# Performance work log

Measured on AMD Instinct MI355X. Metric: run time of the kernel, lower is better.

The kernel has to match this reference:

```python
import jax, jax.numpy as jnp
import numpy as np

K = 2  # binary (k-ary) heap-layout tree: children of node j are K*j+1 .. K*j+K

def _levels(N):
    # level of node i in heap layout = floor(log2(i+1)); returns list of index arrays, root level first
    lev = np.floor(np.log2(np.arange(N) + 1)).astype(np.int64)
    depth = int(lev.max()) + 1
    return [np.where(lev == l)[0] for l in range(depth)]

def setup_inputs() -> dict:
    key = jax.random.key(0)
    ks = jax.random.split(key, 9)
    B, N, D = 512, 127, 300
    s = 0.05
    return {
        'x':     jax.random.normal(ks[0], (B, N, D), jnp.float32),
        'Wioux': jax.random.normal(ks[1], (D, 3 * D), jnp.float32) * s,
        'bioux': jax.random.normal(ks[2], (3 * D,), jnp.float32) * s,
        'Wiouh': jax.random.normal(ks[3], (D, 3 * D), jnp.float32) * s,
        'biouh': jax.random.normal(ks[4], (3 * D,), jnp.float32) * s,
        'Wfx':   jax.random.normal(ks[5], (D, D), jnp.float32) * s,
        'bfx':   jax.random.normal(ks[6], (D,), jnp.float32) * s,
        'Wfh':   jax.random.normal(ks[7], (D, D), jnp.float32) * s,
        'bfh':   jax.random.normal(ks[8], (D,), jnp.float32) * s,
    }

def reference(x, Wioux, bioux, Wiouh, biouh, Wfx, bfx, Wfh, bfh):
    # Child-Sum Tree-LSTM, level-synchronous (leaves -> root), batched over B trees.
    B, N, D = x.shape
    levels = _levels(N)
    H = jnp.zeros((B, N, D), x.dtype)
    C = jnp.zeros((B, N, D), x.dtype)
    for idx in reversed(levels):  # process deepest level first
        ch = idx[:, None] * K + 1 + np.arange(K)          # [n, K] child node ids (static)
        valid = jnp.asarray((ch < N), x.dtype)[None, :, :, None]  # [1,n,K,1]
        chc = np.minimum(ch, N - 1)
        ch_h = H[:, chc] * valid                           # [B,n,K,D]; padded children -> 0 (leaf case)
        ch_c = C[:, chc] * valid
        h_sum = ch_h.sum(axis=2)                           # child-sum of hidden states [B,n,D]
        xj = x[:, idx]                                     # [B,n,D]
        iou = xj @ Wioux + bioux + h_sum @ Wiouh + biouh   # [B,n,3D]
        i_g, o_g, u_g = jnp.split(iou, 3, axis=-1)
        i_g = jax.nn.sigmoid(i_g)
        o_g = jax.nn.sigmoid(o_g)
        u_g = jnp.tanh(u_g)
        fx = (xj @ Wfx + bfx)[:, :, None, :]               # broadcast over children
        f = jax.nn.sigmoid(jnp.einsum('bnkd,de->bnke', ch_h, Wfh) + bfh + fx)
        c = i_g * u_g + (f * ch_c).sum(axis=2)             # fc sum; padded ch_c==0
        h = o_g * jnp.tanh(c)
        H = H.at[:, idx].set(h)
        C = C.at[:, idx].set(c)
    return H  # per-node hidden states (contexts); root hidden = H[:, 0]
```

## Files before the change

### kernel.cpp

```cpp
#include <hip/hip_runtime.h>
#include <math.h>

#define DIM 300
#define NN 127
#define KP 320
#define MATSZ (KP*KP)

typedef short bf16x8 __attribute__((ext_vector_type(8)));
typedef float f32x16 __attribute__((ext_vector_type(16)));

__device__ __forceinline__ unsigned short f2bf(float f){
    unsigned u = __float_as_uint(f);
    u += 0x7fffu + ((u >> 16) & 1u);
    return (unsigned short)(u >> 16);
}
__device__ __forceinline__ float sigf(float v){ return 1.0f/(1.0f+__expf(-v)); }
__device__ __forceinline__ float tanh_(float v){
    float t = __expf(-2.0f*fabsf(v));
    float r = (1.0f - t)/(1.0f + t);
    return v < 0.0f ? -r : r;
}
__device__ __forceinline__ void glds16(const void* g, void* l){
    __builtin_amdgcn_global_load_lds(
        (const __attribute__((address_space(1))) unsigned int*)g,
        (__attribute__((address_space(3))) unsigned int*)l, 16, 0, 0);
}

#define MFMA __builtin_amdgcn_mfma_f32_32x32x16_bf16

__global__ void prep_weights(const float* __restrict__ Wioux,
                             const float* __restrict__ Wiouh,
                             const float* __restrict__ Wfx,
                             const float* __restrict__ Wfh,
                             unsigned short* __restrict__ WT)
{
    int k = threadIdx.x;
    int n = blockIdx.x;
    int m = blockIdx.y;
    float v = 0.f;
    if (k < DIM && n < DIM){
        if (m < 3)       v = Wioux[k*(3*DIM) + m*DIM + n];
        else if (m < 6)  v = Wiouh[k*(3*DIM) + (m-3)*DIM + n];
        else if (m == 6) v = Wfx[k*DIM + n];
        else             v = Wfh[k*DIM + n];
    }
    WT[m*MATSZ + n*KP + k] = f2bf(v);
}

__global__ __launch_bounds__(256,2)
void leaf_mfma(const float* __restrict__ x,
               const float* __restrict__ bioux, const float* __restrict__ biouh,
               const unsigned short* __restrict__ WT,
               float* __restrict__ H, float* __restrict__ C)
{
    __shared__ __attribute__((aligned(16))) short lds[10240];
    const int t = threadIdx.x, lane = t & 63, wave = t >> 6;
    const int wm = wave >> 1, wn = wave & 1;
    const int lrow = lane & 31, half = lane >> 5;
    const int rowBase = blockIdx.x * 128, d0 = blockIdx.y * 64;

    const float* aptr[2]; int adst[2]; int acg[2];
    #pragma unroll
    for (int i = 0; i < 2; i++){
        int ca = wave*2 + i;
        int r = ca*16 + (lane >> 2);
        int grow = rowBase + r;
        int b = grow >> 6, j = 63 + (grow & 63);
        int cg = (lane & 3) ^ (r & 3);
        aptr[i] = x + (b*NN + j)*DIM + cg*8;
        acg[i] = cg;
        adst[i] = ca*512 + lane*8;
    }
    const unsigned short* bptr[3]; short* bdst[3];
    #pragma unroll
    for (int i = 0; i < 3; i++){
        int cb = wave*3 + i;
        int m = cb >> 2, g = cb & 3;
        int n = g*16 + (lane >> 2);
        int cg = (lane & 3) ^ (n & 3);
        bptr[i] = WT + m*MATSZ + (d0 + n)*KP + cg*8;
        bdst[i] = lds + 4096 + cb*512;
    }

    f32x16 accI[2], accO[2], accU[2];
    #pragma unroll
    for (int rt = 0; rt < 2; rt++)
        #pragma unroll
        for (int q = 0; q < 16; q++){ accI[rt][q]=0.f; accO[rt][q]=0.f; accU[rt][q]=0.f; }

    #pragma unroll
    for (int ks = 0; ks < 10; ks++){
        #pragma unroll
        for (int i = 0; i < 3; i++) glds16(bptr[i] + ks*32, bdst[i]);
        #pragma unroll
        for (int i = 0; i < 2; i++){
            bf16x8 v;
            if ((ks+1)*32 <= DIM){
                float4 p0 = *(const float4*)(aptr[i] + ks*32);
                float4 p1 = *(const float4*)(aptr[i] + ks*32 + 4);
                v[0]=f2bf(p0.x); v[1]=f2bf(p0.y); v[2]=f2bf(p0.z); v[3]=f2bf(p0.w);
                v[4]=f2bf(p1.x); v[5]=f2bf(p1.y); v[6]=f2bf(p1.z); v[7]=f2bf(p1.w);
            } else {
                int kc = ks*32 + acg[i]*8;
                #pragma unroll
                for (int e = 0; e < 8; e++) v[e] = 0;
                if (kc + 8 <= DIM){
                    float4 p0 = *(const float4*)(aptr[i] + ks*32);
                    float4 p1 = *(const float4*)(aptr[i] + ks*32 + 4);
                    v[0]=f2bf(p0.x); v[1]=f2bf(p0.y); v[2]=f2bf(p0.z); v[3]=f2bf(p0.w);
                    v[4]=f2bf(p1.x); v[5]=f2bf(p1.y); v[6]=f2bf(p1.z); v[7]=f2bf(p1.w);
                } else if (kc < DIM){
                    float4 p0 = *(const float4*)(aptr[i] + ks*32);
                    v[0]=f2bf(p0.x); v[1]=f2bf(p0.y); v[2]=f2bf(p0.z); v[3]=f2bf(p0.w);
                }
            }
            *(bf16x8*)(lds + adst[i]) = v;
        }
        __syncthreads();
        #pragma unroll
        for (int kk = 0; kk < 2; kk++){
            int p = ((kk<<1) + half) ^ (lrow & 3);
            const short* Bb = lds + 4096 + (wn*32 + lrow)*32 + p*8;
            bf16x8 b0 = *(const bf16x8*)(Bb);
            bf16x8 b1 = *(const bf16x8*)(Bb + 2048);
            bf16x8 b2 = *(const bf16x8*)(Bb + 4096);
            const short* Ab = lds + (wm*64 + lrow)*32 + p*8;
            #pragma unroll
            for (int rt = 0; rt < 2; rt++){
                bf16x8 ax = *(const bf16x8*)(Ab + rt*1024);
                accI[rt] = MFMA(ax, b0, accI[rt], 0, 0, 0);
                accO[rt] = MFMA(ax, b1, accO[rt], 0, 0, 0);
                accU[rt] = MFMA(ax, b2, accU[rt], 0, 0, 0);
            }
        }
        __syncthreads();
    }
    int d = d0 + wn*32 + lrow;
    if (d < DIM){
        float bi  = bioux[d]       + biouh[d];
        float bo_ = bioux[DIM+d]   + biouh[DIM+d];
        float bu  = bioux[2*DIM+d] + biouh[2*DIM+d];
        #pragma unroll
        for (int rt = 0; rt < 2; rt++)
            #pragma unroll
            for (int q = 0; q < 16; q++){
                int grow = rowBase + wm*64 + rt*32 + (q&3) + 8*(q>>2) + 4*half;
                int b = grow >> 6, j = 63 + (grow & 63);
                int ob = (b*NN + j)*DIM + d;
                float iv = sigf (accI[rt][q] + bi);
                float ov = sigf (accO[rt][q] + bo_);
                float uv = tanh_(accU[rt][q] + bu);
                float cv = iv*uv;
                C[ob] = cv;
                H[ob] = ov*tanh_(cv);
            }
    }
}

__global__ __launch_bounds__(256,2)
void level_mfma(const float* __restrict__ x,
                const float* __restrict__ bioux, const float* __restrict__ biouh,
                const float* __restrict__ bfx,   const float* __restrict__ bfh,
                const unsigned short* __restrict__ WT,
                float* __restrict__ H, float* __restrict__ C,
                int lo, int lshift)
{
    __shared__ __attribute__((aligned(16))) short lds[28672];
    const int t = threadIdx.x, lane = t & 63, wave = t >> 6;
    const int wm = wave >> 1, wn = wave & 1;
    const int lrow = lane & 31, half = lane >> 5;
    const int rowBase = blockIdx.x * 128, d0 = blockIdx.y * 64;
    const int nmask = (1 << lshift) - 1;

    const float* aptr[6]; int adst[6]; int acg[6];
    #pragma unroll
    for (int i = 0; i < 6; i++){
        int ca = wave*6 + i;
        int s = ca >> 3, rg = ca & 7;
        int r = rg*16 + (lane >> 2);
        int grow = rowBase + r;
        int b = grow >> lshift, j = lo + (grow & nmask);
        int node = (s == 0) ? j : ((s == 1) ? 2*j+1 : 2*j+2);
        const float* base = (s == 0) ? x : H;
        int cg = (lane & 3) ^ (r & 3);
        aptr[i] = base + (b*NN + node)*DIM + cg*8;
        acg[i] = cg;
        adst[i] = ca*512 + lane*8;
    }
    const unsigned short* bptr[8]; short* bdst[8];
    #pragma unroll
    for (int i = 0; i < 8; i++){
        int cb = wave*8 + i;
        int m = cb >> 2, g = cb & 3;
        int n = g*16 + (lane >> 2);
        int cg = (lane & 3) ^ (n & 3);
        bptr[i] = WT + m*MATSZ + (d0 + n)*KP + cg*8;
        bdst[i] = lds + 12288 + cb*512;
    }

    f32x16 accI[2], accO[2], accU[2], accF0[2], accF1[2];
    #pragma unroll
    for (int rt = 0; rt < 2; rt++)
        #pragma unroll
        for (int q = 0; q < 16; q++){
            accI[rt][q]=0.f; accO[rt][q]=0.f; accU[rt][q]=0.f;
            accF0[rt][q]=0.f; accF1[rt][q]=0.f;
        }

    #pragma unroll
    for (int ks = 0; ks < 10; ks++){
        #pragma unroll
        for (int i = 0; i < 8; i++) glds16(bptr[i] + ks*32, bdst[i]);
        #pragma unroll
        for (int i = 0; i < 6; i++){
            bf16x8 v;
            if ((ks+1)*32 <= DIM){
                float4 p0 = *(const float4*)(aptr[i] + ks*32);
                float4 p1 = *(const float4*)(aptr[i] + ks*32 + 4);
                v[0]=f2bf(p0.x); v[1]=f2bf(p0.y); v[2]=f2bf(p0.z); v[3]=f2bf(p0.w);
                v[4]=f2bf(p1.x); v[5]=f2bf(p1.y); v[6]=f2bf(p1.z); v[7]=f2bf(p1.w);
            } else {
                int kc = ks*32 + acg[i]*8;
                #pragma unroll
                for (int e = 0; e < 8; e++) v[e] = 0;
                if (kc + 8 <= DIM){
                    float4 p0 = *(const float4*)(aptr[i] + ks*32);
                    float4 p1 = *(const float4*)(aptr[i] + ks*32 + 4);
                    v[0]=f2bf(p0.x); v[1]=f2bf(p0.y); v[2]=f2bf(p0.z); v[3]=f2bf(p0.w);
                    v[4]=f2bf(p1.x); v[5]=f2bf(p1.y); v[6]=f2bf(p1.z); v[7]=f2bf(p1.w);
                } else if (kc < DIM){
                    float4 p0 = *(const float4*)(aptr[i] + ks*32);
                    v[0]=f2bf(p0.x); v[1]=f2bf(p0.y); v[2]=f2bf(p0.z); v[3]=f2bf(p0.w);
                }
            }
            *(bf16x8*)(lds + adst[i]) = v;
        }
        __syncthreads();
        #pragma unroll
        for (int kk = 0; kk < 2; kk++){
            int p = ((kk<<1) + half) ^ (lrow & 3);
            const short* Bb = lds + 12288 + (wn*32 + lrow)*32 + p*8;
            bf16x8 b0 = *(const bf16x8*)(Bb);
            bf16x8 b1 = *(const bf16x8*)(Bb + 2048);
            bf16x8 b2 = *(const bf16x8*)(Bb + 2*2048);
            bf16x8 b3 = *(const bf16x8*)(Bb + 3*2048);
            bf16x8 b4 = *(const bf16x8*)(Bb + 4*2048);
            bf16x8 b5 = *(const bf16x8*)(Bb + 5*2048);
            bf16x8 b6 = *(const bf16x8*)(Bb + 6*2048);
            bf16x8 b7 = *(const bf16x8*)(Bb + 7*2048);
            const short* Ab = lds + (wm*64 + lrow)*32 + p*8;
            #pragma unroll
            for (int rt = 0; rt < 2; rt++){
                bf16x8 ax = *(const bf16x8*)(Ab + rt*1024);
                bf16x8 a0 = *(const bf16x8*)(Ab + 4096 + rt*1024);
                bf16x8 a1 = *(const bf16x8*)(Ab + 8192 + rt*1024);
                accI[rt]  = MFMA(ax, b0, accI[rt], 0, 0, 0);
                accI[rt]  = MFMA(a0, b3, accI[rt], 0, 0, 0);
                accI[rt]  = MFMA(a1, b3, accI[rt], 0, 0, 0);
                accO[rt]  = MFMA(ax, b1, accO[rt], 0, 0, 0);
                accO[rt]  = MFMA(a0, b4, accO[rt], 0, 0, 0);
                accO[rt]  = MFMA(a1, b4, accO[rt], 0, 0, 0);
                accU[rt]  = MFMA(ax, b2, accU[rt], 0, 0, 0);
                accU[rt]  = MFMA(a0, b5, accU[rt], 0, 0, 0);
                accU[rt]  = MFMA(a1, b5, accU[rt], 0, 0, 0);
                accF0[rt] = MFMA(ax, b6, accF0[rt], 0, 0, 0);
                accF0[rt] = MFMA(a0, b7, accF0[rt], 0, 0, 0);
                accF1[rt] = MFMA(ax, b6, accF1[rt], 0, 0, 0);
                accF1[rt] = MFMA(a1, b7, accF1[rt], 0, 0, 0);
            }
        }
        __syncthreads();
    }
    int d = d0 + wn*32 + lrow;
    if (d < DIM){
        float bi  = bioux[d]       + biouh[d];
        float bo_ = bioux[DIM+d]   + biouh[DIM+d];
        float bu  = bioux[2*DIM+d] + biouh[2*DIM+d];
        float bf_ = bfx[d] + bfh[d];
        #pragma unroll
        for (int rt = 0; rt < 2; rt++)
            #pragma unroll
            for (int q = 0; q < 16; q++){
                int grow = rowBase + wm*64 + rt*32 + (q&3) + 8*(q>>2) + 4*half;
                int b = grow >> lshift, j = lo + (grow & nmask);
                int ob  = (b*NN + j)*DIM + d;
                float c0 = C[(b*NN + 2*j+1)*DIM + d];
                float c1 = C[(b*NN + 2*j+2)*DIM + d];
                float iv = sigf (accI[rt][q] + bi);
                float ov = sigf (accO[rt][q] + bo_);
                float uv = tanh_(accU[rt][q] + bu);
                float f0 = sigf (accF0[rt][q] + bf_);
                float f1 = sigf (accF1[rt][q] + bf_);
                float cv = iv*uv + f0*c0 + f1*c1;
                C[ob] = cv;
                H[ob] = ov*tanh_(cv);
            }
    }
}

extern "C" void kernel_launch(void* const* d_in, const int* in_sizes, int n_in,
                              void* d_out, int out_size, void* d_ws, size_t ws_size,
                              hipStream_t stream) {
    const float* x     = (const float*)d_in[0];
    const float* Wioux = (const float*)d_in[1];
    const float* bioux = (const float*)d_in[2];
    const float* Wiouh = (const float*)d_in[3];
    const float* biouh = (const float*)d_in[4];
    const float* Wfx   = (const float*)d_in[5];
    const float* bfx   = (const float*)d_in[6];
    const float* Wfh   = (const float*)d_in[7];
    const float* bfh   = (const float*)d_in[8];
    float* H = (float*)d_out;
    float* C = (float*)d_ws;
    unsigned short* WT = (unsigned short*)((char*)d_ws + 78028800);

    prep_weights<<<dim3(KP, 8), KP, 0, stream>>>(Wioux, Wiouh, Wfx, Wfh, WT);
    leaf_mfma<<<dim3(256, 5), 256, 0, stream>>>(x, bioux, biouh, WT, H, C);
    for (int l = 5; l >= 0; l--){
        level_mfma<<<dim3(4 << l, 5), 256, 0, stream>>>(
            x, bioux, biouh, bfx, bfh, WT, H, C, (1 << l) - 1, l);
    }
}
```

Measured before the change: 604.1 us.

## Pre-convert x and hidden states to padded bf16; load MFMA operands directly from global

Adds a prep_x kernel that converts all of x to bf16 with rows padded to 320, and has each level kernel also write a padded bf16 copy of H. The MFMA kernels drop LDS staging and __syncthreads and read A and B fragments straight from global memory in their register layout. This removes the per-block fp32-to-bf16 conversion, the boundary handling and the barriers. In exchange it adds a full extra pass over x plus bf16 H stores, and gives up LDS reuse of the weight tiles, so operands are re-read from L2 or global by every wave. The workspace offsets must also fit the new buffers.

```diff
diff --git a/kernel.cpp b/kernel.cpp
--- a/kernel.cpp
+++ b/kernel.cpp
@@ -19,11 +19,6 @@
     float t = __expf(-2.0f*fabsf(v));
     float r = (1.0f - t)/(1.0f + t);
     return v < 0.0f ? -r : r;
-}
-__device__ __forceinline__ void glds16(const void* g, void* l){
-    __builtin_amdgcn_global_load_lds(
-        (const __attribute__((address_space(1))) unsigned int*)g,
-        (__attribute__((address_space(3))) unsigned int*)l, 16, 0, 0);
 }
 
 #define MFMA __builtin_amdgcn_mfma_f32_32x32x16_bf16
@@ -47,40 +42,34 @@
     WT[m*MATSZ + n*KP + k] = f2bf(v);
 }
 
+__global__ void prep_x(const float* __restrict__ x, unsigned short* __restrict__ xbf)
+{
+    int row = blockIdx.x;
+    int t = threadIdx.x;
+    float v = (t < DIM) ? x[row*DIM + t] : 0.f;
+    xbf[row*KP + t] = f2bf(v);
+}
+
 __global__ __launch_bounds__(256,2)
-void leaf_mfma(const float* __restrict__ x,
+void leaf_mfma(const unsigned short* __restrict__ xbf,
                const float* __restrict__ bioux, const float* __restrict__ biouh,
                const unsigned short* __restrict__ WT,
-               float* __restrict__ H, float* __restrict__ C)
-{
-    __shared__ __attribute__((aligned(16))) short lds[10240];
+               float* __restrict__ H, float* __restrict__ C,
+               unsigned short* __restrict__ hbf)
+{
     const int t = threadIdx.x, lane = t & 63, wave = t >> 6;
     const int wm = wave >> 1, wn = wave & 1;
     const int lrow = lane & 31, half = lane >> 5;
     const int rowBase = blockIdx.x * 128, d0 = blockIdx.y * 64;
 
-    const float* aptr[2]; int adst[2]; int acg[2];
-    #pragma unroll
-    for (int i = 0; i < 2; i++){
-        int ca = wave*2 + i;
-        int r = ca*16 + (lane >> 2);
-        int grow = rowBase + r;
+    const unsigned short* xr[2];
+    #pragma unroll
+    for (int rt = 0; rt < 2; rt++){
+        int grow = rowBase + wm*64 + rt*32 + lrow;
         int b = grow >> 6, j = 63 + (grow & 63);
-        int cg = (lane & 3) ^ (r & 3);
-        aptr[i] = x + (b*NN + j)*DIM + cg*8;
-        acg[i] = cg;
-        adst[i] = ca*512 + lane*8;
-    }
-    const unsigned short* bptr[3]; short* bdst[3];
-    #pragma unroll
-    for (int i = 0; i < 3; i++){
-        int cb = wave*3 + i;
-        int m = cb >> 2, g = cb & 3;
-        int n = g*16 + (lane >> 2);
-        int cg = (lane & 3) ^ (n & 3);
-        bptr[i] = WT + m*MATSZ + (d0 + n)*KP + cg*8;
-        bdst[i] = lds + 4096 + cb*512;
-    }
+        xr[rt] = xbf + (b*NN + j)*KP + half*8;
+    }
+    const unsigned short* wb = WT + (d0 + wn*32 + lrow)*KP + half*8;
 
     f32x16 accI[2], accO[2], accU[2];
     #pragma unroll
@@ -91,49 +80,19 @@
     #pragma unroll
     for (int ks = 0; ks < 10; ks++){
         #pragma unroll
-        for (int i = 0; i < 3; i++) glds16(bptr[i] + ks*32, bdst[i]);
-        #pragma unroll
-        for (int i = 0; i < 2; i++){
-            bf16x8 v;
-            if ((ks+1)*32 <= DIM){
-                float4 p0 = *(const float4*)(aptr[i] + ks*32);
-                float4 p1 = *(const float4*)(aptr[i] + ks*32 + 4);
-                v[0]=f2bf(p0.x); v[1]=f2bf(p0.y); v[2]=f2bf(p0.z); v[3]=f2bf(p0.w);
-                v[4]=f2bf(p1.x); v[5]=f2bf(p1.y); v[6]=f2bf(p1.z); v[7]=f2bf(p1.w);
-            } else {
-                int kc = ks*32 + acg[i]*8;
-                #pragma unroll
-                for (int e = 0; e < 8; e++) v[e] = 0;
-                if (kc + 8 <= DIM){
-                    float4 p0 = *(const float4*)(aptr[i] + ks*32);
-                    float4 p1 = *(const float4*)(aptr[i] + ks*32 + 4);
-                    v[0]=f2bf(p0.x); v[1]=f2bf(p0.y); v[2]=f2bf(p0.z); v[3]=f2bf(p0.w);
-                    v[4]=f2bf(p1.x); v[5]=f2bf(p1.y); v[6]=f2bf(p1.z); v[7]=f2bf(p1.w);
-                } else if (kc < DIM){
-                    float4 p0 = *(const float4*)(aptr[i] + ks*32);
-                    v[0]=f2bf(p0.x); v[1]=f2bf(p0.y); v[2]=f2bf(p0.z); v[3]=f2bf(p0.w);
-                }
-            }
-            *(bf16x8*)(lds + adst[i]) = v;
-        }
-        __syncthreads();
-        #pragma unroll
         for (int kk = 0; kk < 2; kk++){
-            int p = ((kk<<1) + half) ^ (lrow & 3);
-            const short* Bb = lds + 4096 + (wn*32 + lrow)*32 + p*8;
-            bf16x8 b0 = *(const bf16x8*)(Bb);
-            bf16x8 b1 = *(const bf16x8*)(Bb + 2048);
-            bf16x8 b2 = *(const bf16x8*)(Bb + 4096);
-            const short* Ab = lds + (wm*64 + lrow)*32 + p*8;
+            const int off = ks*32 + kk*16;
+            bf16x8 b0 = *(const bf16x8*)(wb + 0*MATSZ + off);
+            bf16x8 b1 = *(const bf16x8*)(wb + 1*MATSZ + off);
+            bf16x8 b2 = *(const bf16x8*)(wb + 2*MATSZ + off);
             #pragma unroll
             for (int rt = 0; rt < 2; rt++){
-                bf16x8 ax = *(const bf16x8*)(Ab + rt*1024);
+                bf16x8 ax = *(const bf16x8*)(xr[rt] + off);
                 accI[rt] = MFMA(ax, b0, accI[rt], 0, 0, 0);
                 accO[rt] = MFMA(ax, b1, accO[rt], 0, 0, 0);
                 accU[rt] = MFMA(ax, b2, accU[rt], 0, 0, 0);
             }
         }
-        __syncthreads();
     }
     int d = d0 + wn*32 + lrow;
     if (d < DIM){
@@ -146,57 +105,45 @@
             for (int q = 0; q < 16; q++){
                 int grow = rowBase + wm*64 + rt*32 + (q&3) + 8*(q>>2) + 4*half;
                 int b = grow >> 6, j = 63 + (grow & 63);
-                int ob = (b*NN + j)*DIM + d;
+                int nb = b*NN + j;
                 float iv = sigf (accI[rt][q] + bi);
                 float ov = sigf (accO[rt][q] + bo_);
                 float uv = tanh_(accU[rt][q] + bu);
                 float cv = iv*uv;
-                C[ob] = cv;
-                H[ob] = ov*tanh_(cv);
+                float hv = ov*tanh_(cv);
+                C[nb*DIM + d] = cv;
+                H[nb*DIM + d] = hv;
+                hbf[nb*KP + d] = f2bf(hv);
             }
     }
 }
 
 __global__ __launch_bounds__(256,2)
-void level_mfma(const float* __restrict__ x,
+void level_mfma(const unsigned short* __restrict__ xbf,
+                const unsigned short* __restrict__ hbf,
                 const float* __restrict__ bioux, const float* __restrict__ biouh,
                 const float* __restrict__ bfx,   const float* __restrict__ bfh,
                 const unsigned short* __restrict__ WT,
                 float* __restrict__ H, float* __restrict__ C,
+                unsigned short* __restrict__ hbf_out,
                 int lo, int lshift)
 {
-    __shared__ __attribute__((aligned(16))) short lds[28672];
     const int t = threadIdx.x, lane = t & 63, wave = t >> 6;
     const int wm = wave >> 1, wn = wave & 1;
     const int lrow = lane & 31, half = lane >> 5;
     const int rowBase = blockIdx.x * 128, d0 = blockIdx.y * 64;
     const int nmask = (1 << lshift) - 1;
 
-    const float* aptr[6]; int adst[6]; int acg[6];
-    #pragma unroll
-    for (int i = 0; i < 6; i++){
-        int ca = wave*6 + i;
-        int s = ca >> 3, rg = ca & 7;
-        int r = rg*16 + (lane >> 2);
-        int grow = rowBase + r;
+    const unsigned short *xr[2], *h0r[2], *h1r[2];
+    #pragma unroll
+    for (int rt = 0; rt < 2; rt++){
+        int grow = rowBase + wm*64 + rt*32 + lrow;
         int b = grow >> lshift, j = lo + (grow & nmask);
-        int node = (s == 0) ? j : ((s == 1) ? 2*j+1 : 2*j+2);
-        const float* base = (s == 0) ? x : H;
-        int cg = (lane & 3) ^ (r & 3);
-        aptr[i] = base + (b*NN + node)*DIM + cg*8;
-        acg[i] = cg;
-        adst[i] = ca*512 + lane*8;
-    }
-    const unsigned short* bptr[8]; short* bdst[8];
-    #pragma unroll
-    for (int i = 0; i < 8; i++){
-        int cb = wave*8 + i;
-        int m = cb >> 2, g = cb & 3;
-        int n = g*16 + (lane >> 2);
-        int cg = (lane & 3) ^ (n & 3);
-        bptr[i] = WT + m*MATSZ + (d0 + n)*KP + cg*8;
-        bdst[i] = lds + 12288 + cb*512;
-    }
+        xr[rt]  = xbf + (b*NN + j)*KP + half*8;
+        h0r[rt] = hbf + (b*NN + 2*j+1)*KP + half*8;
+        h1r[rt] = hbf + (b*NN + 2*j+2)*KP + half*8;
+    }
+    const unsigned short* wb = WT + (d0 + wn*32 + lrow)*KP + half*8;
 
     f32x16 accI[2], accO[2], accU[2], accF0[2], accF1[2];
     #pragma unroll
@@ -210,50 +157,21 @@
     #pragma unroll
     for (int ks = 0; ks < 10; ks++){
         #pragma unroll
-        for (int i = 0; i < 8; i++) glds16(bptr[i] + ks*32, bdst[i]);
-        #pragma unroll
-        for (int i = 0; i < 6; i++){
-            bf16x8 v;
-            if ((ks+1)*32 <= DIM){
-                float4 p0 = *(const float4*)(aptr[i] + ks*32);
-                float4 p1 = *(const float4*)(aptr[i] + ks*32 + 4);
-                v[0]=f2bf(p0.x); v[1]=f2bf(p0.y); v[2]=f2bf(p0.z); v[3]=f2bf(p0.w);
-                v[4]=f2bf(p1.x); v[5]=f2bf(p1.y); v[6]=f2bf(p1.z); v[7]=f2bf(p1.w);
-            } else {
-                int kc = ks*32 + acg[i]*8;
-                #pragma unroll
-                for (int e = 0; e < 8; e++) v[e] = 0;
-                if (kc + 8 <= DIM){
-                    float4 p0 = *(const float4*)(aptr[i] + ks*32);
-                    float4 p1 = *(const float4*)(aptr[i] + ks*32 + 4);
-                    v[0]=f2bf(p0.x); v[1]=f2bf(p0.y); v[2]=f2bf(p0.z); v[3]=f2bf(p0.w);
-                    v[4]=f2bf(p1.x); v[5]=f2bf(p1.y); v[6]=f2bf(p1.z); v[7]=f2bf(p1.w);
-                } else if (kc < DIM){
-                    float4 p0 = *(const float4*)(aptr[i] + ks*32);
-                    v[0]=f2bf(p0.x); v[1]=f2bf(p0.y); v[2]=f2bf(p0.z); v[3]=f2bf(p0.w);
-                }
-            }
-            *(bf16x8*)(lds + adst[i]) = v;
-        }
-        __syncthreads();
-        #pragma unroll
         for (int kk = 0; kk < 2; kk++){
-            int p = ((kk<<1) + half) ^ (lrow & 3);
-            const short* Bb = lds + 12288 + (wn*32 + lrow)*32 + p*8;
-            bf16x8 b0 = *(const bf16x8*)(Bb);
-            bf16x8 b1 = *(const bf16x8*)(Bb + 2048);
-            bf16x8 b2 = *(const bf16x8*)(Bb + 2*2048);
-            bf16x8 b3 = *(const bf16x8*)(Bb + 3*2048);
-            bf16x8 b4 = *(const bf16x8*)(Bb + 4*2048);
-            bf16x8 b5 = *(const bf16x8*)(Bb + 5*2048);
-            bf16x8 b6 = *(const bf16x8*)(Bb + 6*2048);
-            bf16x8 b7 = *(const bf16x8*)(Bb + 7*2048);
-            const short* Ab = lds + (wm*64 + lrow)*32 + p*8;
+            const int off = ks*32 + kk*16;
+            bf16x8 b0 = *(const bf16x8*)(wb + 0*MATSZ + off);
+            bf16x8 b1 = *(const bf16x8*)(wb + 1*MATSZ + off);
+            bf16x8 b2 = *(const bf16x8*)(wb + 2*MATSZ + off);
+            bf16x8 b3 = *(const bf16x8*)(wb + 3*MATSZ + off);
+            bf16x8 b4 = *(const bf16x8*)(wb + 4*MATSZ + off);
+            bf16x8 b5 = *(const bf16x8*)(wb + 5*MATSZ + off);
+            bf16x8 b6 = *(const bf16x8*)(wb + 6*MATSZ + off);
+            bf16x8 b7 = *(const bf16x8*)(wb + 7*MATSZ + off);
             #pragma unroll
             for (int rt = 0; rt < 2; rt++){
-                bf16x8 ax = *(const bf16x8*)(Ab + rt*1024);
-                bf16x8 a0 = *(const bf16x8*)(Ab + 4096 + rt*1024);
-                bf16x8 a1 = *(const bf16x8*)(Ab + 8192 + rt*1024);
+                bf16x8 ax = *(const bf16x8*)(xr[rt]  + off);
+                bf16x8 a0 = *(const bf16x8*)(h0r[rt] + off);
+                bf16x8 a1 = *(const bf16x8*)(h1r[rt] + off);
                 accI[rt]  = MFMA(ax, b0, accI[rt], 0, 0, 0);
                 accI[rt]  = MFMA(a0, b3, accI[rt], 0, 0, 0);
                 accI[rt]  = MFMA(a1, b3, accI[rt], 0, 0, 0);
@@ -269,7 +187,6 @@
                 accF1[rt] = MFMA(a1, b7, accF1[rt], 0, 0, 0);
             }
         }
-        __syncthreads();
     }
     int d = d0 + wn*32 + lrow;
     if (d < DIM){
@@ -283,7 +200,7 @@
             for (int q = 0; q < 16; q++){
                 int grow = rowBase + wm*64 + rt*32 + (q&3) + 8*(q>>2) + 4*half;
                 int b = grow >> lshift, j = lo + (grow & nmask);
-                int ob  = (b*NN + j)*DIM + d;
+                int nb = b*NN + j;
                 float c0 = C[(b*NN + 2*j+1)*DIM + d];
                 float c1 = C[(b*NN + 2*j+2)*DIM + d];
                 float iv = sigf (accI[rt][q] + bi);
@@ -292,8 +209,10 @@
                 float f0 = sigf (accF0[rt][q] + bf_);
                 float f1 = sigf (accF1[rt][q] + bf_);
                 float cv = iv*uv + f0*c0 + f1*c1;
-                C[ob] = cv;
-                H[ob] = ov*tanh_(cv);
+                float hv = ov*tanh_(cv);
+                C[nb*DIM + d] = cv;
+                H[nb*DIM + d] = hv;
+                hbf_out[nb*KP + d] = f2bf(hv);
             }
     }
 }
@@ -312,12 +231,15 @@
     const float* bfh   = (const float*)d_in[8];
     float* H = (float*)d_out;
     float* C = (float*)d_ws;
-    unsigned short* WT = (unsigned short*)((char*)d_ws + 78028800);
+    unsigned short* WT  = (unsigned short*)((char*)d_ws + 78028800);
+    unsigned short* xbf = (unsigned short*)((char*)d_ws + 79667200);
+    unsigned short* hbf = (unsigned short*)((char*)d_ws + 121282560);
 
     prep_weights<<<dim3(KP, 8), KP, 0, stream>>>(Wioux, Wiouh, Wfx, Wfh, WT);
-    leaf_mfma<<<dim3(256, 5), 256, 0, stream>>>(x, bioux, biouh, WT, H, C);
+    prep_x<<<dim3(512*NN), KP, 0, stream>>>(x, xbf);
+    leaf_mfma<<<dim3(256, 5), 256, 0, stream>>>(xbf, bioux, biouh, WT, H, C, hbf);
     for (int l = 5; l >= 0; l--){
         level_mfma<<<dim3(4 << l, 5), 256, 0, stream>>>(
-            x, bioux, biouh, bfx, bfh, WT, H, C, (1 << l) - 1, l);
-    }
-}
+            xbf, hbf, bioux, biouh, bfx, bfh, WT, H, C, hbf, (1 << l) - 1, l);
+    }
+}
```

Measured after the change: 716.3 us. 1.19x slower.
